# Kernel tuning notes

Measured on AMD Instinct MI355X. Metric: run time of the kernel, lower is better.

The kernel has to match this reference:

```python
import jax, jax.numpy as jnp
import numpy as np

B = 256
N_SNP = 100000
BITS = 4          # snp_onehot_bits
BLOCK = 20        # SNPs per block
N_BLOCKS = N_SNP // BLOCK            # 5000 output blocks
IN_DIM = N_SNP * BITS                # 400000
DIMS = [1024, 256]
OUT_DIM = 1
LN_EPS = 1e-5


def _make_indices():
    # blocks_gt[i] = [20*i, ..., 20*i+19]; replicate get_param4sparse
    blocks = np.arange(N_SNP, dtype=np.int64).reshape(N_BLOCKS, BLOCK)
    idx0 = (blocks[:, :, None] * BITS + np.arange(BITS)).reshape(-1)   # input bit index, [nnz]
    idx1 = np.repeat(np.arange(N_BLOCKS, dtype=np.int64), BLOCK * BITS)  # output block index, [nnz]
    return jnp.asarray(idx0, jnp.int32), jnp.asarray(idx1, jnp.int32)


def setup_inputs() -> dict:
    key = jax.random.key(0)
    ks = jax.random.split(key, 9)
    idx0, idx1 = _make_indices()
    x = jax.random.uniform(ks[0], (B, IN_DIM), dtype=jnp.float32)
    sparse_values = jax.random.normal(ks[1], (idx0.shape[0],), dtype=jnp.float32)
    ln_gamma = jnp.ones((N_BLOCKS,), jnp.float32)
    ln_beta = jnp.zeros((N_BLOCKS,), jnp.float32)
    s1 = 1.0 / np.sqrt(N_BLOCKS)
    W1 = jax.random.uniform(ks[2], (DIMS[0], N_BLOCKS), jnp.float32, -s1, s1)
    b1 = jax.random.uniform(ks[3], (DIMS[0],), jnp.float32, -s1, s1)
    s2 = 1.0 / np.sqrt(DIMS[0])
    W2 = jax.random.uniform(ks[4], (DIMS[1], DIMS[0]), jnp.float32, -s2, s2)
    b2 = jax.random.uniform(ks[5], (DIMS[1],), jnp.float32, -s2, s2)
    s3 = 1.0 / np.sqrt(DIMS[1])
    W3 = jax.random.uniform(ks[6], (OUT_DIM, DIMS[1]), jnp.float32, -s3, s3)
    b3 = jax.random.uniform(ks[7], (OUT_DIM,), jnp.float32, -s3, s3)
    return {"x": x, "sparse_values": sparse_values, "ln_gamma": ln_gamma,
            "ln_beta": ln_beta, "W1": W1, "b1": b1, "W2": W2, "b2": b2,
            "W3": W3, "b3": b3, "idx0": idx0, "idx1": idx1}


def reference(x, sparse_values, ln_gamma, ln_beta, W1, b1, W2, b2, W3, b3, idx0, idx1):
    # SparseLinear: out[b, j] = sum_{k: idx1[k]==j} sparse_values[k] * x[b, idx0[k]]
    gathered = x[:, idx0] * sparse_values[None, :]                       # [B, nnz]
    gblocks = jax.ops.segment_sum(gathered.T, idx1, num_segments=N_BLOCKS).T  # [B, n_blocks]
    # LayerNorm over block dim
    mu = jnp.mean(gblocks, axis=-1, keepdims=True)
    var = jnp.mean(jnp.square(gblocks - mu), axis=-1, keepdims=True)
    h = (gblocks - mu) * jax.lax.rsqrt(var + LN_EPS) * ln_gamma + ln_beta
    # Dense head (note: no activation after first Linear, faithful to source)
    h = h @ W1.T + b1
    h = h @ W2.T + b2
    h = jax.nn.sigmoid(h)
    return h @ W3.T + b3                                                 # [B, OUT_DIM]
```

## Files before the change

kernel.cpp:

```cpp
#include <hip/hip_runtime.h>
#include <math.h>

#define BATCH   256
#define NBLK    5000
#define NBLKP   5024
#define IN_DIM  400000
#define D1      1024
#define D2      256
#define K1P     5120
#define NSPLIT  16
#define ZK      (K1P / NSPLIT)
#define ZSTEPS  (ZK / 64)

typedef __attribute__((ext_vector_type(8))) short short8_t;
typedef __attribute__((ext_vector_type(4))) float f32x4;

static __device__ __forceinline__ unsigned short f2bf(float f) {
    union { float f; unsigned int u; } v; v.f = f;
    unsigned int u = v.u;
    return (unsigned short)((u + 0x7FFFu + ((u >> 16) & 1u)) >> 16);
}

__global__ __launch_bounds__(256) void k_sparse(const float* __restrict__ x,
                                                const float* __restrict__ sv,
                                                float* __restrict__ g) {
    __shared__ float xs[64 * 84];
    const int bx  = blockIdx.x;
    const int b   = blockIdx.y;
    const int tid = threadIdx.x;
    const int gidx = tid >> 2;
    const int s    = tid & 3;
    const int j    = bx * 64 + gidx;
    const bool jv  = (j < NBLK);

    float4 sva[5];
    if (jv) {
        const float4* sr = reinterpret_cast<const float4*>(sv + (size_t)j * 80);
#pragma unroll
        for (int r = 0; r < 5; ++r) sva[r] = sr[r * 4 + s];
    }

    const float* xrow = x + (size_t)b * IN_DIM + (size_t)bx * 5120;
    const int fmax = 100000 - bx * 1280;
#pragma unroll
    for (int i = 0; i < 5; ++i) {
        const int f = tid + i * 256;
        if (f < fmax) {
            const float4 v = *reinterpret_cast<const float4*>(xrow + f * 4);
            const int jl = f / 20;
            const int m  = f % 20;
            *reinterpret_cast<float4*>(&xs[jl * 84 + m * 4]) = v;
        }
    }
    __syncthreads();

    if (!jv) return;
    const float4* xl = reinterpret_cast<const float4*>(&xs[gidx * 84]);
    float acc = 0.0f;
#pragma unroll
    for (int r = 0; r < 5; ++r) {
        const float4 xv = xl[r * 4 + s];
        const float4 sg = sva[r];
        acc += xv.x * sg.x + xv.y * sg.y + xv.z * sg.z + xv.w * sg.w;
    }
    acc += __shfl_xor(acc, 1);
    acc += __shfl_xor(acc, 2);
    if (s == 0) g[(size_t)b * NBLKP + j] = acc;
}

__global__ __launch_bounds__(256) void k_ln(const float* __restrict__ g,
                                            const float* __restrict__ gamma,
                                            const float* __restrict__ beta,
                                            unsigned short* __restrict__ A) {
    const int b   = blockIdx.x;
    const int tid = threadIdx.x;
    const float* row = g + (size_t)b * NBLKP;
    float4 v[5];
    float s = 0.0f, ss = 0.0f;
#pragma unroll
    for (int i = 0; i < 5; ++i) {
        const int f4 = tid + i * 256;
        float4 vv = {0.f, 0.f, 0.f, 0.f};
        if (f4 < 1250) vv = *reinterpret_cast<const float4*>(row + f4 * 4);
        v[i] = vv;
        s  += vv.x + vv.y + vv.z + vv.w;
        ss += vv.x * vv.x + vv.y * vv.y + vv.z * vv.z + vv.w * vv.w;
    }
#pragma unroll
    for (int o = 32; o > 0; o >>= 1) {
        s  += __shfl_xor(s, o);
        ss += __shfl_xor(ss, o);
    }
    __shared__ float ls[4], lss[4];
    const int wid = tid >> 6;
    if ((tid & 63) == 0) { ls[wid] = s; lss[wid] = ss; }
    __syncthreads();
    s  = ls[0] + ls[1] + ls[2] + ls[3];
    ss = lss[0] + lss[1] + lss[2] + lss[3];
    const float mu  = s / (float)NBLK;
    const float var = ss / (float)NBLK - mu * mu;
    const float rs  = rsqrtf(var + 1e-5f);
    unsigned short* dst = A + (size_t)b * K1P;
#pragma unroll
    for (int i = 0; i < 5; ++i) {
        const int f4 = tid + i * 256;
        if (f4 < 1280) {
            const int c = f4 * 4;
            ushort4 o;
            if (f4 < 1250) {
                const float4 gm = *reinterpret_cast<const float4*>(gamma + c);
                const float4 bt = *reinterpret_cast<const float4*>(beta + c);
                o = { f2bf((v[i].x - mu) * rs * gm.x + bt.x),
                      f2bf((v[i].y - mu) * rs * gm.y + bt.y),
                      f2bf((v[i].z - mu) * rs * gm.z + bt.z),
                      f2bf((v[i].w - mu) * rs * gm.w + bt.w) };
            } else {
                o = ushort4{0, 0, 0, 0};
            }
            *reinterpret_cast<ushort4*>(dst + c) = o;
        }
    }
}

__global__ __launch_bounds__(256) void k_gemm1(const unsigned short* __restrict__ A,
                                               const float* __restrict__ W1,
                                               float* __restrict__ C) {
    const int n0 = blockIdx.x * 64;
    const int z  = blockIdx.y;
    const int kbase = z * ZK;
    float* Cz = C + (size_t)z * BATCH * D1;

    __shared__ unsigned short As[256][72];
    __shared__ unsigned short Ws[64][72];

    const int tid  = threadIdx.x;
    const int wave = tid >> 6;
    const int lane = tid & 63;
    const int lr   = lane & 15;
    const int lk   = (lane >> 4) * 8;
    const int srow = tid >> 3;
    const int scol = (tid & 7) * 8;
    const int wrow = tid >> 2;
    const int wcol = (tid & 3) * 16;

    const unsigned short* Ap = A + (size_t)srow * K1P + kbase + scol;
    const float* Wrow = W1 + (size_t)(n0 + wrow) * NBLK;

    short8_t pa[8];
    float4 pwf[4];
    auto loadA = [&](int t) {
#pragma unroll
        for (int it = 0; it < 8; ++it)
            pa[it] = *reinterpret_cast<const short8_t*>(Ap + (size_t)it * 32 * K1P + t * 64);
    };
    auto loadW = [&](int t) {
        const int k0 = kbase + t * 64 + wcol;
#pragma unroll
        for (int q = 0; q < 4; ++q) {
            const int k = k0 + q * 4;
            pwf[q] = (k < NBLK) ? *reinterpret_cast<const float4*>(Wrow + k)
                                : float4{0.f, 0.f, 0.f, 0.f};
        }
    };

    loadA(0);
    loadW(0);

    f32x4 acc[4][4] = {};

    for (int t = 0; t < ZSTEPS; ++t) {
        __syncthreads();
#pragma unroll
        for (int it = 0; it < 8; ++it)
            *reinterpret_cast<short8_t*>(&As[srow + it * 32][scol]) = pa[it];
        {
            short8_t w0 = { (short)f2bf(pwf[0].x), (short)f2bf(pwf[0].y), (short)f2bf(pwf[0].z), (short)f2bf(pwf[0].w),
                            (short)f2bf(pwf[1].x), (short)f2bf(pwf[1].y), (short)f2bf(pwf[1].z), (short)f2bf(pwf[1].w) };
            short8_t w1 = { (short)f2bf(pwf[2].x), (short)f2bf(pwf[2].y), (short)f2bf(pwf[2].z), (short)f2bf(pwf[2].w),
                            (short)f2bf(pwf[3].x), (short)f2bf(pwf[3].y), (short)f2bf(pwf[3].z), (short)f2bf(pwf[3].w) };
            *reinterpret_cast<short8_t*>(&Ws[wrow][wcol])     = w0;
            *reinterpret_cast<short8_t*>(&Ws[wrow][wcol + 8]) = w1;
        }
        __syncthreads();
        if (t + 1 < ZSTEPS) { loadA(t + 1); loadW(t + 1); }
#pragma unroll
        for (int kk = 0; kk < 64; kk += 32) {
            short8_t a[4], bf[4];
#pragma unroll
            for (int i = 0; i < 4; ++i)
                a[i] = *reinterpret_cast<const short8_t*>(&As[wave * 64 + i * 16 + lr][kk + lk]);
#pragma unroll
            for (int jj = 0; jj < 4; ++jj)
                bf[jj] = *reinterpret_cast<const short8_t*>(&Ws[jj * 16 + lr][kk + lk]);
#pragma unroll
            for (int i = 0; i < 4; ++i)
#pragma unroll
                for (int jj = 0; jj < 4; ++jj)
                    acc[i][jj] = __builtin_amdgcn_mfma_f32_16x16x32_bf16(a[i], bf[jj], acc[i][jj], 0, 0, 0);
        }
    }

    const int rbase = (lane >> 4) * 4;
#pragma unroll
    for (int i = 0; i < 4; ++i)
#pragma unroll
        for (int jj = 0; jj < 4; ++jj) {
            const int col = n0 + jj * 16 + lr;
#pragma unroll
            for (int r = 0; r < 4; ++r) {
                const int row = wave * 64 + i * 16 + rbase + r;
                Cz[(size_t)row * D1 + col] = acc[i][jj][r];
            }
        }
}

__global__ __launch_bounds__(256) void k_fuse(const float* __restrict__ p,
                                              const float* __restrict__ b1,
                                              unsigned short* __restrict__ A2,
                                              const float* __restrict__ W2,
                                              unsigned short* __restrict__ W2b) {
    const int idx = (blockIdx.x * 256 + threadIdx.x) * 4;
    const int col = idx & (D1 - 1);
    const size_t S = (size_t)BATCH * D1;
    float4 bb = *reinterpret_cast<const float4*>(b1 + col);
    float sx = bb.x, sy = bb.y, sz = bb.z, sw = bb.w;
#pragma unroll
    for (int q = 0; q < NSPLIT; ++q) {
        float4 v = *reinterpret_cast<const float4*>(p + q * S + idx);
        sx += v.x; sy += v.y; sz += v.z; sw += v.w;
    }
    ushort4 o = { f2bf(sx), f2bf(sy), f2bf(sz), f2bf(sw) };
    *reinterpret_cast<ushort4*>(A2 + idx) = o;
    float4 wv = *reinterpret_cast<const float4*>(W2 + idx);
    ushort4 wo = { f2bf(wv.x), f2bf(wv.y), f2bf(wv.z), f2bf(wv.w) };
    *reinterpret_cast<ushort4*>(W2b + idx) = wo;
}

__global__ __launch_bounds__(512) void k_tail(const unsigned short* __restrict__ A2,
                                              const unsigned short* __restrict__ W2b,
                                              const float* __restrict__ b2,
                                              const float* __restrict__ W3,
                                              const float* __restrict__ b3,
                                              float* __restrict__ out) {
    const int m0 = blockIdx.x * 32;
    __shared__ unsigned short As[32][72];
    __shared__ unsigned short Ws[256][72];
    __shared__ float red[8][32];

    const int tid  = threadIdx.x;
    const int wave = tid >> 6;
    const int lane = tid & 63;
    const int wc   = wave * 32;
    const int lr   = lane & 15;
    const int lk   = (lane >> 4) * 8;
    const int srow = tid >> 3;
    const int scol = (tid & 7) * 8;

    const unsigned short* Ap = A2 + (size_t)(m0 + srow) * D1 + scol;
    const unsigned short* Wp = W2b + (size_t)srow * D1 + scol;

    short8_t pa = {};
    short8_t pw[4];
    if (tid < 256) pa = *reinterpret_cast<const short8_t*>(Ap);
#pragma unroll
    for (int it = 0; it < 4; ++it)
        pw[it] = *reinterpret_cast<const short8_t*>(Wp + (size_t)it * 64 * D1);

    f32x4 acc[2][2] = {};

    for (int t = 0; t < 16; ++t) {
        __syncthreads();
        if (tid < 256) *reinterpret_cast<short8_t*>(&As[srow][scol]) = pa;
#pragma unroll
        for (int it = 0; it < 4; ++it)
            *reinterpret_cast<short8_t*>(&Ws[srow + it * 64][scol]) = pw[it];
        __syncthreads();
        if (t + 1 < 16) {
            const int ko = (t + 1) * 64;
            if (tid < 256) pa = *reinterpret_cast<const short8_t*>(Ap + ko);
#pragma unroll
            for (int it = 0; it < 4; ++it)
                pw[it] = *reinterpret_cast<const short8_t*>(Wp + (size_t)it * 64 * D1 + ko);
        }
#pragma unroll
        for (int kk = 0; kk < 64; kk += 32) {
            short8_t a0 = *reinterpret_cast<const short8_t*>(&As[lr][kk + lk]);
            short8_t a1 = *reinterpret_cast<const short8_t*>(&As[16 + lr][kk + lk]);
#pragma unroll
            for (int j = 0; j < 2; ++j) {
                short8_t bj = *reinterpret_cast<const short8_t*>(&Ws[wc + j * 16 + lr][kk + lk]);
                acc[0][j] = __builtin_amdgcn_mfma_f32_16x16x32_bf16(a0, bj, acc[0][j], 0, 0, 0);
                acc[1][j] = __builtin_amdgcn_mfma_f32_16x16x32_bf16(a1, bj, acc[1][j], 0, 0, 0);
            }
        }
    }

    float b2c[2], w3c[2];
#pragma unroll
    for (int j = 0; j < 2; ++j) {
        const int col = wc + j * 16 + lr;
        b2c[j] = b2[col];
        w3c[j] = W3[col];
    }
    const int rbase = (lane >> 4) * 4;
#pragma unroll
    for (int i = 0; i < 2; ++i) {
#pragma unroll
        for (int r = 0; r < 4; ++r) {
            float pv = 0.0f;
#pragma unroll
            for (int j = 0; j < 2; ++j) {
                const float h = acc[i][j][r] + b2c[j];
                pv += w3c[j] / (1.0f + __expf(-h));
            }
            pv += __shfl_xor(pv, 1);
            pv += __shfl_xor(pv, 2);
            pv += __shfl_xor(pv, 4);
            pv += __shfl_xor(pv, 8);
            if (lr == 0) red[wave][i * 16 + rbase + r] = pv;
        }
    }
    __syncthreads();
    if (tid < 32) {
        float s2 = 0.0f;
#pragma unroll
        for (int w = 0; w < 8; ++w) s2 += red[w][tid];
        out[m0 + tid] = s2 + b3[0];
    }
}

extern "C" void kernel_launch(void* const* d_in, const int* in_sizes, int n_in,
                              void* d_out, int out_size, void* d_ws, size_t ws_size,
                              hipStream_t stream) {
    const float* x     = (const float*)d_in[0];
    const float* sv    = (const float*)d_in[1];
    const float* gamma = (const float*)d_in[2];
    const float* beta  = (const float*)d_in[3];
    const float* W1    = (const float*)d_in[4];
    const float* b1    = (const float*)d_in[5];
    const float* W2    = (const float*)d_in[6];
    const float* b2    = (const float*)d_in[7];
    const float* W3    = (const float*)d_in[8];
    const float* b3    = (const float*)d_in[9];
    float* out = (float*)d_out;

    char* ws = (char*)d_ws;
    size_t off = 0;
    auto alloc = [&](size_t bytes) { char* p = ws + off; off = (off + bytes + 255) & ~(size_t)255; return p; };
    float*          g     = (float*)         alloc((size_t)BATCH * NBLKP * 4);
    unsigned short* Ab    = (unsigned short*)alloc((size_t)BATCH * K1P * 2);
    float*          out1p = (float*)         alloc((size_t)NSPLIT * BATCH * D1 * 4);
    unsigned short* A2b   = (unsigned short*)alloc((size_t)BATCH * D1 * 2);
    unsigned short* W2b   = (unsigned short*)alloc((size_t)D2 * D1 * 2);

    k_sparse<<<dim3((NBLK + 63) / 64, BATCH), 256, 0, stream>>>(x, sv, g);
    k_ln<<<dim3(BATCH), 256, 0, stream>>>(g, gamma, beta, Ab);
    k_gemm1<<<dim3(D1 / 64, NSPLIT), 256, 0, stream>>>(Ab, W1, out1p);
    k_fuse<<<dim3(BATCH * D1 / (256 * 4)), 256, 0, stream>>>(out1p, b1, A2b, W2, W2b);
    k_tail<<<dim3(BATCH / 8), 512, 0, stream>>>(A2b, W2b, b2, W3, b3, out);
}
```

Baseline: 128.5 us.

## Fold LayerNorm algebraically into GEMM1 and drop the separate LN kernel

The separate LayerNorm kernel is removed. k_sparse now emits per-block partial sums and sums of squares. GEMM1 consumes the raw fp32 block outputs, scales W1 by gamma, and accumulates per-column terms sum(gamma*W1) and sum(beta*W1), so the mean and rstd are applied afterwards in k_fuse as rs*(s - mu*t) + u. This saves a kernel launch and a round trip of the normalized activations through memory. The cost is extra gamma/beta loads and conversions inside the GEMM loop, more registers (launch_bounds min 1), and bf16 rounding of raw rather than normalized activations, which may change precision.

```diff
diff --git a/kernel.cpp b/kernel.cpp
--- a/kernel.cpp
+++ b/kernel.cpp
@@ -11,6 +11,7 @@
 #define NSPLIT  16
 #define ZK      (K1P / NSPLIT)
 #define ZSTEPS  (ZK / 64)
+#define NBX     ((NBLK + 63) / 64)
 
 typedef __attribute__((ext_vector_type(8))) short short8_t;
 typedef __attribute__((ext_vector_type(4))) float f32x4;
@@ -20,11 +21,18 @@
     unsigned int u = v.u;
     return (unsigned short)((u + 0x7FFFu + ((u >> 16) & 1u)) >> 16);
 }
+static __device__ __forceinline__ short8_t cvt8(const float4& a, const float4& b) {
+    short8_t r = { (short)f2bf(a.x), (short)f2bf(a.y), (short)f2bf(a.z), (short)f2bf(a.w),
+                   (short)f2bf(b.x), (short)f2bf(b.y), (short)f2bf(b.z), (short)f2bf(b.w) };
+    return r;
+}
 
 __global__ __launch_bounds__(256) void k_sparse(const float* __restrict__ x,
                                                 const float* __restrict__ sv,
-                                                float* __restrict__ g) {
+                                                float* __restrict__ g,
+                                                float2* __restrict__ part) {
     __shared__ float xs[64 * 84];
+    __shared__ float2 pr[4];
     const int bx  = blockIdx.x;
     const int b   = blockIdx.y;
     const int tid = threadIdx.x;
@@ -54,77 +62,43 @@
     }
     __syncthreads();
 
-    if (!jv) return;
-    const float4* xl = reinterpret_cast<const float4*>(&xs[gidx * 84]);
     float acc = 0.0f;
-#pragma unroll
-    for (int r = 0; r < 5; ++r) {
-        const float4 xv = xl[r * 4 + s];
-        const float4 sg = sva[r];
-        acc += xv.x * sg.x + xv.y * sg.y + xv.z * sg.z + xv.w * sg.w;
+    if (jv) {
+        const float4* xl = reinterpret_cast<const float4*>(&xs[gidx * 84]);
+#pragma unroll
+        for (int r = 0; r < 5; ++r) {
+            const float4 xv = xl[r * 4 + s];
+            const float4 sg = sva[r];
+            acc += xv.x * sg.x + xv.y * sg.y + xv.z * sg.z + xv.w * sg.w;
+        }
     }
     acc += __shfl_xor(acc, 1);
     acc += __shfl_xor(acc, 2);
-    if (s == 0) g[(size_t)b * NBLKP + j] = acc;
-}
-
-__global__ __launch_bounds__(256) void k_ln(const float* __restrict__ g,
-                                            const float* __restrict__ gamma,
-                                            const float* __restrict__ beta,
-                                            unsigned short* __restrict__ A) {
-    const int b   = blockIdx.x;
-    const int tid = threadIdx.x;
-    const float* row = g + (size_t)b * NBLKP;
-    float4 v[5];
-    float s = 0.0f, ss = 0.0f;
-#pragma unroll
-    for (int i = 0; i < 5; ++i) {
-        const int f4 = tid + i * 256;
-        float4 vv = {0.f, 0.f, 0.f, 0.f};
-        if (f4 < 1250) vv = *reinterpret_cast<const float4*>(row + f4 * 4);
-        v[i] = vv;
-        s  += vv.x + vv.y + vv.z + vv.w;
-        ss += vv.x * vv.x + vv.y * vv.y + vv.z * vv.z + vv.w * vv.w;
-    }
+    if (s == 0 && jv) g[(size_t)b * NBLKP + j] = acc;
+
+    float sm = (s == 0 && jv) ? acc : 0.0f;
+    float sq = sm * sm;
 #pragma unroll
     for (int o = 32; o > 0; o >>= 1) {
-        s  += __shfl_xor(s, o);
-        ss += __shfl_xor(ss, o);
-    }
-    __shared__ float ls[4], lss[4];
-    const int wid = tid >> 6;
-    if ((tid & 63) == 0) { ls[wid] = s; lss[wid] = ss; }
+        sm += __shfl_xor(sm, o);
+        sq += __shfl_xor(sq, o);
+    }
+    if ((tid & 63) == 0) pr[tid >> 6] = float2{sm, sq};
     __syncthreads();
-    s  = ls[0] + ls[1] + ls[2] + ls[3];
-    ss = lss[0] + lss[1] + lss[2] + lss[3];
-    const float mu  = s / (float)NBLK;
-    const float var = ss / (float)NBLK - mu * mu;
-    const float rs  = rsqrtf(var + 1e-5f);
-    unsigned short* dst = A + (size_t)b * K1P;
-#pragma unroll
-    for (int i = 0; i < 5; ++i) {
-        const int f4 = tid + i * 256;
-        if (f4 < 1280) {
-            const int c = f4 * 4;
-            ushort4 o;
-            if (f4 < 1250) {
-                const float4 gm = *reinterpret_cast<const float4*>(gamma + c);
-                const float4 bt = *reinterpret_cast<const float4*>(beta + c);
-                o = { f2bf((v[i].x - mu) * rs * gm.x + bt.x),
-                      f2bf((v[i].y - mu) * rs * gm.y + bt.y),
-                      f2bf((v[i].z - mu) * rs * gm.z + bt.z),
-                      f2bf((v[i].w - mu) * rs * gm.w + bt.w) };
-            } else {
-                o = ushort4{0, 0, 0, 0};
-            }
-            *reinterpret_cast<ushort4*>(dst + c) = o;
-        }
-    }
-}
-
-__global__ __launch_bounds__(256) void k_gemm1(const unsigned short* __restrict__ A,
-                                               const float* __restrict__ W1,
-                                               float* __restrict__ C) {
+    if (tid == 0) {
+        float2 t = {pr[0].x + pr[1].x + pr[2].x + pr[3].x,
+                    pr[0].y + pr[1].y + pr[2].y + pr[3].y};
+        part[b * 80 + bx] = t;
+    }
+}
+
+__global__ __launch_bounds__(256, 1) void k_gemm1(const float* __restrict__ g,
+                                                  const float* __restrict__ W1,
+                                                  const float* __restrict__ gamma,
+                                                  const float* __restrict__ beta,
+                                                  float* __restrict__ C,
+                                                  float* __restrict__ T1p,
+                                                  float* __restrict__ U1p) {
     const int n0 = blockIdx.x * 64;
     const int z  = blockIdx.y;
     const int kbase = z * ZK;
@@ -143,23 +117,37 @@
     const int wrow = tid >> 2;
     const int wcol = (tid & 3) * 16;
 
-    const unsigned short* Ap = A + (size_t)srow * K1P + kbase + scol;
+    const float* Gp   = g + (size_t)srow * NBLKP + kbase + scol;
     const float* Wrow = W1 + (size_t)(n0 + wrow) * NBLK;
 
-    short8_t pa[8];
-    float4 pwf[4];
+    float4 pa[16];
+    float4 pw[4], pg[4], pb[4];
+
     auto loadA = [&](int t) {
 #pragma unroll
-        for (int it = 0; it < 8; ++it)
-            pa[it] = *reinterpret_cast<const short8_t*>(Ap + (size_t)it * 32 * K1P + t * 64);
+        for (int it = 0; it < 8; ++it) {
+            const int k0 = kbase + t * 64 + scol;
+            const float* base = Gp + (size_t)it * 32 * NBLKP + t * 64;
+            pa[it * 2]     = (k0 < NBLK)     ? *reinterpret_cast<const float4*>(base)
+                                             : float4{0.f, 0.f, 0.f, 0.f};
+            pa[it * 2 + 1] = (k0 + 4 < NBLK) ? *reinterpret_cast<const float4*>(base + 4)
+                                             : float4{0.f, 0.f, 0.f, 0.f};
+        }
     };
     auto loadW = [&](int t) {
         const int k0 = kbase + t * 64 + wcol;
 #pragma unroll
         for (int q = 0; q < 4; ++q) {
             const int k = k0 + q * 4;
-            pwf[q] = (k < NBLK) ? *reinterpret_cast<const float4*>(Wrow + k)
-                                : float4{0.f, 0.f, 0.f, 0.f};
+            if (k < NBLK) {
+                pw[q] = *reinterpret_cast<const float4*>(Wrow + k);
+                pg[q] = *reinterpret_cast<const float4*>(gamma + k);
+                pb[q] = *reinterpret_cast<const float4*>(beta + k);
+            } else {
+                pw[q] = float4{0.f, 0.f, 0.f, 0.f};
+                pg[q] = float4{0.f, 0.f, 0.f, 0.f};
+                pb[q] = float4{0.f, 0.f, 0.f, 0.f};
+            }
         }
     };
 
@@ -167,19 +155,24 @@
     loadW(0);
 
     f32x4 acc[4][4] = {};
+    float t1a = 0.f, u1a = 0.f;
 
     for (int t = 0; t < ZSTEPS; ++t) {
         __syncthreads();
 #pragma unroll
         for (int it = 0; it < 8; ++it)
-            *reinterpret_cast<short8_t*>(&As[srow + it * 32][scol]) = pa[it];
+            *reinterpret_cast<short8_t*>(&As[srow + it * 32][scol]) = cvt8(pa[it * 2], pa[it * 2 + 1]);
         {
-            short8_t w0 = { (short)f2bf(pwf[0].x), (short)f2bf(pwf[0].y), (short)f2bf(pwf[0].z), (short)f2bf(pwf[0].w),
-                            (short)f2bf(pwf[1].x), (short)f2bf(pwf[1].y), (short)f2bf(pwf[1].z), (short)f2bf(pwf[1].w) };
-            short8_t w1 = { (short)f2bf(pwf[2].x), (short)f2bf(pwf[2].y), (short)f2bf(pwf[2].z), (short)f2bf(pwf[2].w),
-                            (short)f2bf(pwf[3].x), (short)f2bf(pwf[3].y), (short)f2bf(pwf[3].z), (short)f2bf(pwf[3].w) };
-            *reinterpret_cast<short8_t*>(&Ws[wrow][wcol])     = w0;
-            *reinterpret_cast<short8_t*>(&Ws[wrow][wcol + 8]) = w1;
+            float4 pr[4];
+#pragma unroll
+            for (int q = 0; q < 4; ++q) {
+                pr[q].x = pg[q].x * pw[q].x; pr[q].y = pg[q].y * pw[q].y;
+                pr[q].z = pg[q].z * pw[q].z; pr[q].w = pg[q].w * pw[q].w;
+                t1a += pr[q].x + pr[q].y + pr[q].z + pr[q].w;
+                u1a += pb[q].x * pw[q].x + pb[q].y * pw[q].y + pb[q].z * pw[q].z + pb[q].w * pw[q].w;
+            }
+            *reinterpret_cast<short8_t*>(&Ws[wrow][wcol])     = cvt8(pr[0], pr[1]);
+            *reinterpret_cast<short8_t*>(&Ws[wrow][wcol + 8]) = cvt8(pr[2], pr[3]);
         }
         __syncthreads();
         if (t + 1 < ZSTEPS) { loadA(t + 1); loadW(t + 1); }
@@ -198,6 +191,13 @@
                 for (int jj = 0; jj < 4; ++jj)
                     acc[i][jj] = __builtin_amdgcn_mfma_f32_16x16x32_bf16(a[i], bf[jj], acc[i][jj], 0, 0, 0);
         }
+    }
+
+    t1a += __shfl_xor(t1a, 1); t1a += __shfl_xor(t1a, 2);
+    u1a += __shfl_xor(u1a, 1); u1a += __shfl_xor(u1a, 2);
+    if ((tid & 3) == 0) {
+        T1p[z * D1 + n0 + wrow] = t1a;
+        U1p[z * D1 + n0 + wrow] = u1a;
     }
 
     const int rbase = (lane >> 4) * 4;
@@ -215,22 +215,52 @@
 }
 
 __global__ __launch_bounds__(256) void k_fuse(const float* __restrict__ p,
+                                              const float2* __restrict__ part,
+                                              const float* __restrict__ T1p,
+                                              const float* __restrict__ U1p,
                                               const float* __restrict__ b1,
                                               unsigned short* __restrict__ A2,
                                               const float* __restrict__ W2,
                                               unsigned short* __restrict__ W2b) {
-    const int idx = (blockIdx.x * 256 + threadIdx.x) * 4;
-    const int col = idx & (D1 - 1);
-    const size_t S = (size_t)BATCH * D1;
+    __shared__ float ls[4], lss[4];
+    const int b   = blockIdx.x;
+    const int tid = threadIdx.x;
+
+    float2 pv = (tid < NBX) ? part[b * 80 + tid] : float2{0.f, 0.f};
+    float sm = pv.x, sq = pv.y;
+#pragma unroll
+    for (int o = 32; o > 0; o >>= 1) {
+        sm += __shfl_xor(sm, o);
+        sq += __shfl_xor(sq, o);
+    }
+    if ((tid & 63) == 0) { ls[tid >> 6] = sm; lss[tid >> 6] = sq; }
+    __syncthreads();
+    const float S  = ls[0] + ls[1] + ls[2] + ls[3];
+    const float SS = lss[0] + lss[1] + lss[2] + lss[3];
+    const float mu = S / (float)NBLK;
+    const float var = SS / (float)NBLK - mu * mu;
+    const float rs  = rsqrtf(var + 1e-5f);
+
+    const int col = tid * 4;
+    const size_t S2 = (size_t)BATCH * D1;
+    float4 s1 = {0.f, 0.f, 0.f, 0.f}, t1 = {0.f, 0.f, 0.f, 0.f}, u1 = {0.f, 0.f, 0.f, 0.f};
+#pragma unroll
+    for (int z = 0; z < NSPLIT; ++z) {
+        float4 v = *reinterpret_cast<const float4*>(p + z * S2 + (size_t)b * D1 + col);
+        s1.x += v.x; s1.y += v.y; s1.z += v.z; s1.w += v.w;
+        float4 tv = *reinterpret_cast<const float4*>(T1p + z * D1 + col);
+        t1.x += tv.x; t1.y += tv.y; t1.z += tv.z; t1.w += tv.w;
+        float4 uv = *reinterpret_cast<const float4*>(U1p + z * D1 + col);
+        u1.x += uv.x; u1.y += uv.y; u1.z += uv.z; u1.w += uv.w;
+    }
     float4 bb = *reinterpret_cast<const float4*>(b1 + col);
-    float sx = bb.x, sy = bb.y, sz = bb.z, sw = bb.w;
-#pragma unroll
-    for (int q = 0; q < NSPLIT; ++q) {
-        float4 v = *reinterpret_cast<const float4*>(p + q * S + idx);
-        sx += v.x; sy += v.y; sz += v.z; sw += v.w;
-    }
-    ushort4 o = { f2bf(sx), f2bf(sy), f2bf(sz), f2bf(sw) };
-    *reinterpret_cast<ushort4*>(A2 + idx) = o;
+    ushort4 o = { f2bf(rs * (s1.x - mu * t1.x) + u1.x + bb.x),
+                  f2bf(rs * (s1.y - mu * t1.y) + u1.y + bb.y),
+                  f2bf(rs * (s1.z - mu * t1.z) + u1.z + bb.z),
+                  f2bf(rs * (s1.w - mu * t1.w) + u1.w + bb.w) };
+    *reinterpret_cast<ushort4*>(A2 + (size_t)b * D1 + col) = o;
+
+    const int idx = b * D1 + col;
     float4 wv = *reinterpret_cast<const float4*>(W2 + idx);
     ushort4 wo = { f2bf(wv.x), f2bf(wv.y), f2bf(wv.z), f2bf(wv.w) };
     *reinterpret_cast<ushort4*>(W2b + idx) = wo;
@@ -348,14 +378,15 @@
     size_t off = 0;
     auto alloc = [&](size_t bytes) { char* p = ws + off; off = (off + bytes + 255) & ~(size_t)255; return p; };
     float*          g     = (float*)         alloc((size_t)BATCH * NBLKP * 4);
-    unsigned short* Ab    = (unsigned short*)alloc((size_t)BATCH * K1P * 2);
+    float2*         part  = (float2*)        alloc((size_t)BATCH * 80 * 8);
     float*          out1p = (float*)         alloc((size_t)NSPLIT * BATCH * D1 * 4);
+    float*          T1p   = (float*)         alloc((size_t)NSPLIT * D1 * 4);
+    float*          U1p   = (float*)         alloc((size_t)NSPLIT * D1 * 4);
     unsigned short* A2b   = (unsigned short*)alloc((size_t)BATCH * D1 * 2);
     unsigned short* W2b   = (unsigned short*)alloc((size_t)D2 * D1 * 2);
 
-    k_sparse<<<dim3((NBLK + 63) / 64, BATCH), 256, 0, stream>>>(x, sv, g);
-    k_ln<<<dim3(BATCH), 256, 0, stream>>>(g, gamma, beta, Ab);
-    k_gemm1<<<dim3(D1 / 64, NSPLIT), 256, 0, stream>>>(Ab, W1, out1p);
-    k_fuse<<<dim3(BATCH * D1 / (256 * 4)), 256, 0, stream>>>(out1p, b1, A2b, W2, W2b);
+    k_sparse<<<dim3(NBX, BATCH), 256, 0, stream>>>(x, sv, g, part);
+    k_gemm1<<<dim3(D1 / 64, NSPLIT), 256, 0, stream>>>(g, W1, gamma, beta, out1p, T1p, U1p);
+    k_fuse<<<dim3(BATCH), 256, 0, stream>>>(out1p, part, T1p, U1p, b1, A2b, W2, W2b);
     k_tail<<<dim3(BATCH / 8), 512, 0, stream>>>(A2b, W2b, b2, W3, b3, out);
 }
```

Result: slower. 133.6 us (+4.0%).

## Fuse LayerNorm, GEMM1, reduction and tail into one persistent kernel with grid barriers

Applied to the files above, without the earlier changes.

Replaces the four kernels after the sparse gather with a single 256-block persistent kernel. Software grid barriers built on atomic counters separate the LayerNorm, split-K GEMM1, partial-sum reduction and the W2/W3 tail phases. The tail is retiled to 32 blocks of 256 threads, each handling 8 rows padded to 16. This removes launch overhead and inter-kernel gaps, but adds a memset and spin barriers. It relies on all 256 blocks being co-resident, and the tail now uses only 32 blocks with half-empty MFMA tiles.

```diff
diff --git a/kernel.cpp b/kernel.cpp
--- a/kernel.cpp
+++ b/kernel.cpp
@@ -11,6 +11,7 @@
 #define NSPLIT  16
 #define ZK      (K1P / NSPLIT)
 #define ZSTEPS  (ZK / 64)
+#define NBX     ((NBLK + 63) / 64)
 
 typedef __attribute__((ext_vector_type(8))) short short8_t;
 typedef __attribute__((ext_vector_type(4))) float f32x4;
@@ -19,6 +20,19 @@
     union { float f; unsigned int u; } v; v.f = f;
     unsigned int u = v.u;
     return (unsigned short)((u + 0x7FFFu + ((u >> 16) & 1u)) >> 16);
+}
+
+static __device__ __forceinline__ void gridbar(unsigned* cnt, unsigned nblk) {
+    __syncthreads();
+    __threadfence();
+    if (threadIdx.x == 0) {
+        __hip_atomic_fetch_add(cnt, 1u, __ATOMIC_ACQ_REL, __HIP_MEMORY_SCOPE_AGENT);
+        while (__hip_atomic_load(cnt, __ATOMIC_ACQUIRE, __HIP_MEMORY_SCOPE_AGENT) < nblk) {
+            __builtin_amdgcn_s_sleep(2);
+        }
+    }
+    __syncthreads();
+    __threadfence();
 }
 
 __global__ __launch_bounds__(256) void k_sparse(const float* __restrict__ x,
@@ -68,264 +82,255 @@
     if (s == 0) g[(size_t)b * NBLKP + j] = acc;
 }
 
-__global__ __launch_bounds__(256) void k_ln(const float* __restrict__ g,
-                                            const float* __restrict__ gamma,
-                                            const float* __restrict__ beta,
-                                            unsigned short* __restrict__ A) {
-    const int b   = blockIdx.x;
+__global__ __launch_bounds__(256) void k_mega(const float* __restrict__ g,
+                                              const float* __restrict__ gamma,
+                                              const float* __restrict__ beta,
+                                              unsigned short* __restrict__ Ab,
+                                              const float* __restrict__ W1,
+                                              float* __restrict__ out1p,
+                                              const float* __restrict__ b1,
+                                              unsigned short* __restrict__ A2b,
+                                              const float* __restrict__ W2,
+                                              unsigned short* __restrict__ W2b,
+                                              const float* __restrict__ b2,
+                                              const float* __restrict__ W3,
+                                              const float* __restrict__ b3,
+                                              float* __restrict__ out,
+                                              unsigned* __restrict__ bars) {
+    __shared__ char smem[47104];
+    const int blk = blockIdx.x;
     const int tid = threadIdx.x;
-    const float* row = g + (size_t)b * NBLKP;
-    float4 v[5];
-    float s = 0.0f, ss = 0.0f;
-#pragma unroll
-    for (int i = 0; i < 5; ++i) {
-        const int f4 = tid + i * 256;
-        float4 vv = {0.f, 0.f, 0.f, 0.f};
-        if (f4 < 1250) vv = *reinterpret_cast<const float4*>(row + f4 * 4);
-        v[i] = vv;
-        s  += vv.x + vv.y + vv.z + vv.w;
-        ss += vv.x * vv.x + vv.y * vv.y + vv.z * vv.z + vv.w * vv.w;
-    }
-#pragma unroll
-    for (int o = 32; o > 0; o >>= 1) {
-        s  += __shfl_xor(s, o);
-        ss += __shfl_xor(ss, o);
-    }
-    __shared__ float ls[4], lss[4];
-    const int wid = tid >> 6;
-    if ((tid & 63) == 0) { ls[wid] = s; lss[wid] = ss; }
-    __syncthreads();
-    s  = ls[0] + ls[1] + ls[2] + ls[3];
-    ss = lss[0] + lss[1] + lss[2] + lss[3];
-    const float mu  = s / (float)NBLK;
-    const float var = ss / (float)NBLK - mu * mu;
-    const float rs  = rsqrtf(var + 1e-5f);
-    unsigned short* dst = A + (size_t)b * K1P;
-#pragma unroll
-    for (int i = 0; i < 5; ++i) {
-        const int f4 = tid + i * 256;
-        if (f4 < 1280) {
-            const int c = f4 * 4;
-            ushort4 o;
-            if (f4 < 1250) {
-                const float4 gm = *reinterpret_cast<const float4*>(gamma + c);
-                const float4 bt = *reinterpret_cast<const float4*>(beta + c);
-                o = { f2bf((v[i].x - mu) * rs * gm.x + bt.x),
-                      f2bf((v[i].y - mu) * rs * gm.y + bt.y),
-                      f2bf((v[i].z - mu) * rs * gm.z + bt.z),
-                      f2bf((v[i].w - mu) * rs * gm.w + bt.w) };
-            } else {
-                o = ushort4{0, 0, 0, 0};
-            }
-            *reinterpret_cast<ushort4*>(dst + c) = o;
-        }
-    }
-}
-
-__global__ __launch_bounds__(256) void k_gemm1(const unsigned short* __restrict__ A,
-                                               const float* __restrict__ W1,
-                                               float* __restrict__ C) {
-    const int n0 = blockIdx.x * 64;
-    const int z  = blockIdx.y;
-    const int kbase = z * ZK;
-    float* Cz = C + (size_t)z * BATCH * D1;
-
-    __shared__ unsigned short As[256][72];
-    __shared__ unsigned short Ws[64][72];
-
-    const int tid  = threadIdx.x;
     const int wave = tid >> 6;
     const int lane = tid & 63;
     const int lr   = lane & 15;
     const int lk   = (lane >> 4) * 8;
-    const int srow = tid >> 3;
-    const int scol = (tid & 7) * 8;
-    const int wrow = tid >> 2;
-    const int wcol = (tid & 3) * 16;
-
-    const unsigned short* Ap = A + (size_t)srow * K1P + kbase + scol;
-    const float* Wrow = W1 + (size_t)(n0 + wrow) * NBLK;
-
-    short8_t pa[8];
-    float4 pwf[4];
-    auto loadA = [&](int t) {
+
+    {
+        float* ls  = (float*)smem;
+        float* lss = ls + 4;
+        const float* row = g + (size_t)blk * NBLKP;
+        float4 v[5];
+        float s = 0.0f, ss = 0.0f;
+#pragma unroll
+        for (int i = 0; i < 5; ++i) {
+            const int f4 = tid + i * 256;
+            float4 vv = {0.f, 0.f, 0.f, 0.f};
+            if (f4 < 1250) vv = *reinterpret_cast<const float4*>(row + f4 * 4);
+            v[i] = vv;
+            s  += vv.x + vv.y + vv.z + vv.w;
+            ss += vv.x * vv.x + vv.y * vv.y + vv.z * vv.z + vv.w * vv.w;
+        }
+#pragma unroll
+        for (int o = 32; o > 0; o >>= 1) {
+            s  += __shfl_xor(s, o);
+            ss += __shfl_xor(ss, o);
+        }
+        if ((tid & 63) == 0) { ls[tid >> 6] = s; lss[tid >> 6] = ss; }
+        __syncthreads();
+        s  = ls[0] + ls[1] + ls[2] + ls[3];
+        ss = lss[0] + lss[1] + lss[2] + lss[3];
+        const float mu  = s / (float)NBLK;
+        const float var = ss / (float)NBLK - mu * mu;
+        const float rs  = rsqrtf(var + 1e-5f);
+        unsigned short* dst = Ab + (size_t)blk * K1P;
+#pragma unroll
+        for (int i = 0; i < 5; ++i) {
+            const int f4 = tid + i * 256;
+            if (f4 < 1280) {
+                const int c = f4 * 4;
+                ushort4 o;
+                if (f4 < 1250) {
+                    const float4 gm = *reinterpret_cast<const float4*>(gamma + c);
+                    const float4 bt = *reinterpret_cast<const float4*>(beta + c);
+                    o = { f2bf((v[i].x - mu) * rs * gm.x + bt.x),
+                          f2bf((v[i].y - mu) * rs * gm.y + bt.y),
+                          f2bf((v[i].z - mu) * rs * gm.z + bt.z),
+                          f2bf((v[i].w - mu) * rs * gm.w + bt.w) };
+                } else {
+                    o = ushort4{0, 0, 0, 0};
+                }
+                *reinterpret_cast<ushort4*>(dst + c) = o;
+            }
+        }
+    }
+    gridbar(&bars[0], 256);
+
+    {
+        const int n0 = (blk & 15) * 64;
+        const int z  = blk >> 4;
+        const int kbase = z * ZK;
+        float* Cz = out1p + (size_t)z * BATCH * D1;
+
+        auto As = (unsigned short(*)[72])smem;
+        auto Ws = (unsigned short(*)[72])(smem + 36864);
+
+        const int srow = tid >> 3;
+        const int scol = (tid & 7) * 8;
+        const int wrow = tid >> 2;
+        const int wcol = (tid & 3) * 16;
+
+        const unsigned short* Ap = Ab + (size_t)srow * K1P + kbase + scol;
+        const float* Wrow = W1 + (size_t)(n0 + wrow) * NBLK;
+
+        short8_t pa[8];
+        float4 pwf[4];
+        auto loadA = [&](int t) {
+#pragma unroll
+            for (int it = 0; it < 8; ++it)
+                pa[it] = *reinterpret_cast<const short8_t*>(Ap + (size_t)it * 32 * K1P + t * 64);
+        };
+        auto loadW = [&](int t) {
+            const int k0 = kbase + t * 64 + wcol;
+#pragma unroll
+            for (int q = 0; q < 4; ++q) {
+                const int k = k0 + q * 4;
+                pwf[q] = (k < NBLK) ? *reinterpret_cast<const float4*>(Wrow + k)
+                                    : float4{0.f, 0.f, 0.f, 0.f};
+            }
+        };
+
+        loadA(0);
+        loadW(0);
+
+        f32x4 acc[4][4] = {};
+
+        for (int t = 0; t < ZSTEPS; ++t) {
+            __syncthreads();
+#pragma unroll
+            for (int it = 0; it < 8; ++it)
+                *reinterpret_cast<short8_t*>(&As[srow + it * 32][scol]) = pa[it];
+            {
+                short8_t w0 = { (short)f2bf(pwf[0].x), (short)f2bf(pwf[0].y), (short)f2bf(pwf[0].z), (short)f2bf(pwf[0].w),
+                                (short)f2bf(pwf[1].x), (short)f2bf(pwf[1].y), (short)f2bf(pwf[1].z), (short)f2bf(pwf[1].w) };
+                short8_t w1 = { (short)f2bf(pwf[2].x), (short)f2bf(pwf[2].y), (short)f2bf(pwf[2].z), (short)f2bf(pwf[2].w),
+                                (short)f2bf(pwf[3].x), (short)f2bf(pwf[3].y), (short)f2bf(pwf[3].z), (short)f2bf(pwf[3].w) };
+                *reinterpret_cast<short8_t*>(&Ws[wrow][wcol])     = w0;
+                *reinterpret_cast<short8_t*>(&Ws[wrow][wcol + 8]) = w1;
+            }
+            __syncthreads();
+            if (t + 1 < ZSTEPS) { loadA(t + 1); loadW(t + 1); }
+#pragma unroll
+            for (int kk = 0; kk < 64; kk += 32) {
+                short8_t a[4], bf[4];
+#pragma unroll
+                for (int i = 0; i < 4; ++i)
+                    a[i] = *reinterpret_cast<const short8_t*>(&As[wave * 64 + i * 16 + lr][kk + lk]);
+#pragma unroll
+                for (int jj = 0; jj < 4; ++jj)
+                    bf[jj] = *reinterpret_cast<const short8_t*>(&Ws[jj * 16 + lr][kk + lk]);
+#pragma unroll
+                for (int i = 0; i < 4; ++i)
+#pragma unroll
+                    for (int jj = 0; jj < 4; ++jj)
+                        acc[i][jj] = __builtin_amdgcn_mfma_f32_16x16x32_bf16(a[i], bf[jj], acc[i][jj], 0, 0, 0);
+            }
+        }
+
+        const int rbase = (lane >> 4) * 4;
+#pragma unroll
+        for (int i = 0; i < 4; ++i)
+#pragma unroll
+            for (int jj = 0; jj < 4; ++jj) {
+                const int col = n0 + jj * 16 + lr;
+#pragma unroll
+                for (int r = 0; r < 4; ++r) {
+                    const int row = wave * 64 + i * 16 + rbase + r;
+                    Cz[(size_t)row * D1 + col] = acc[i][jj][r];
+                }
+            }
+    }
+    gridbar(&bars[1], 256);
+
+    {
+        const int idx = blk * D1 + tid * 4;
+        const int col = tid * 4;
+        const size_t S2 = (size_t)BATCH * D1;
+        float4 bb = *reinterpret_cast<const float4*>(b1 + col);
+        float sx = bb.x, sy = bb.y, sz = bb.z, sw = bb.w;
+#pragma unroll
+        for (int q = 0; q < NSPLIT; ++q) {
+            float4 v = *reinterpret_cast<const float4*>(out1p + q * S2 + idx);
+            sx += v.x; sy += v.y; sz += v.z; sw += v.w;
+        }
+        ushort4 o = { f2bf(sx), f2bf(sy), f2bf(sz), f2bf(sw) };
+        *reinterpret_cast<ushort4*>(A2b + idx) = o;
+        float4 wv = *reinterpret_cast<const float4*>(W2 + idx);
+        ushort4 wo = { f2bf(wv.x), f2bf(wv.y), f2bf(wv.z), f2bf(wv.w) };
+        *reinterpret_cast<ushort4*>(W2b + idx) = wo;
+    }
+    gridbar(&bars[2], 256);
+
+    if (blk < 32) {
+        const int m0 = blk * 8;
+        auto As2 = (unsigned short(*)[72])smem;
+        auto Ws2 = (unsigned short(*)[72])(smem + 2304);
+        float* red = (float*)(smem + 2304 + 36864);
+
+        const int wc = wave * 64;
+        const int srow = tid >> 3;
+        const int scol = (tid & 7) * 8;
+
+        const unsigned short* Wp = W2b + (size_t)srow * D1 + scol;
+        const unsigned short* Ap = A2b + (size_t)(m0 + (tid >> 3)) * D1 + (tid & 7) * 8;
+
+        short8_t pw[8], pa = {};
 #pragma unroll
         for (int it = 0; it < 8; ++it)
-            pa[it] = *reinterpret_cast<const short8_t*>(Ap + (size_t)it * 32 * K1P + t * 64);
-    };
-    auto loadW = [&](int t) {
-        const int k0 = kbase + t * 64 + wcol;
-#pragma unroll
-        for (int q = 0; q < 4; ++q) {
-            const int k = k0 + q * 4;
-            pwf[q] = (k < NBLK) ? *reinterpret_cast<const float4*>(Wrow + k)
-                                : float4{0.f, 0.f, 0.f, 0.f};
-        }
-    };
-
-    loadA(0);
-    loadW(0);
-
-    f32x4 acc[4][4] = {};
-
-    for (int t = 0; t < ZSTEPS; ++t) {
-        __syncthreads();
-#pragma unroll
-        for (int it = 0; it < 8; ++it)
-            *reinterpret_cast<short8_t*>(&As[srow + it * 32][scol]) = pa[it];
-        {
-            short8_t w0 = { (short)f2bf(pwf[0].x), (short)f2bf(pwf[0].y), (short)f2bf(pwf[0].z), (short)f2bf(pwf[0].w),
-                            (short)f2bf(pwf[1].x), (short)f2bf(pwf[1].y), (short)f2bf(pwf[1].z), (short)f2bf(pwf[1].w) };
-            short8_t w1 = { (short)f2bf(pwf[2].x), (short)f2bf(pwf[2].y), (short)f2bf(pwf[2].z), (short)f2bf(pwf[2].w),
-                            (short)f2bf(pwf[3].x), (short)f2bf(pwf[3].y), (short)f2bf(pwf[3].z), (short)f2bf(pwf[3].w) };
-            *reinterpret_cast<short8_t*>(&Ws[wrow][wcol])     = w0;
-            *reinterpret_cast<short8_t*>(&Ws[wrow][wcol + 8]) = w1;
-        }
-        __syncthreads();
-        if (t + 1 < ZSTEPS) { loadA(t + 1); loadW(t + 1); }
-#pragma unroll
-        for (int kk = 0; kk < 64; kk += 32) {
-            short8_t a[4], bf[4];
-#pragma unroll
-            for (int i = 0; i < 4; ++i)
-                a[i] = *reinterpret_cast<const short8_t*>(&As[wave * 64 + i * 16 + lr][kk + lk]);
-#pragma unroll
-            for (int jj = 0; jj < 4; ++jj)
-                bf[jj] = *reinterpret_cast<const short8_t*>(&Ws[jj * 16 + lr][kk + lk]);
-#pragma unroll
-            for (int i = 0; i < 4; ++i)
-#pragma unroll
-                for (int jj = 0; jj < 4; ++jj)
-                    acc[i][jj] = __builtin_amdgcn_mfma_f32_16x16x32_bf16(a[i], bf[jj], acc[i][jj], 0, 0, 0);
-        }
-    }
-
-    const int rbase = (lane >> 4) * 4;
-#pragma unroll
-    for (int i = 0; i < 4; ++i)
-#pragma unroll
-        for (int jj = 0; jj < 4; ++jj) {
-            const int col = n0 + jj * 16 + lr;
-#pragma unroll
-            for (int r = 0; r < 4; ++r) {
-                const int row = wave * 64 + i * 16 + rbase + r;
-                Cz[(size_t)row * D1 + col] = acc[i][jj][r];
-            }
-        }
-}
-
-__global__ __launch_bounds__(256) void k_fuse(const float* __restrict__ p,
-                                              const float* __restrict__ b1,
-                                              unsigned short* __restrict__ A2,
-                                              const float* __restrict__ W2,
-                                              unsigned short* __restrict__ W2b) {
-    const int idx = (blockIdx.x * 256 + threadIdx.x) * 4;
-    const int col = idx & (D1 - 1);
-    const size_t S = (size_t)BATCH * D1;
-    float4 bb = *reinterpret_cast<const float4*>(b1 + col);
-    float sx = bb.x, sy = bb.y, sz = bb.z, sw = bb.w;
-#pragma unroll
-    for (int q = 0; q < NSPLIT; ++q) {
-        float4 v = *reinterpret_cast<const float4*>(p + q * S + idx);
-        sx += v.x; sy += v.y; sz += v.z; sw += v.w;
-    }
-    ushort4 o = { f2bf(sx), f2bf(sy), f2bf(sz), f2bf(sw) };
-    *reinterpret_cast<ushort4*>(A2 + idx) = o;
-    float4 wv = *reinterpret_cast<const float4*>(W2 + idx);
-    ushort4 wo = { f2bf(wv.x), f2bf(wv.y), f2bf(wv.z), f2bf(wv.w) };
-    *reinterpret_cast<ushort4*>(W2b + idx) = wo;
-}
-
-__global__ __launch_bounds__(512) void k_tail(const unsigned short* __restrict__ A2,
-                                              const unsigned short* __restrict__ W2b,
-                                              const float* __restrict__ b2,
-                                              const float* __restrict__ W3,
-                                              const float* __restrict__ b3,
-                                              float* __restrict__ out) {
-    const int m0 = blockIdx.x * 32;
-    __shared__ unsigned short As[32][72];
-    __shared__ unsigned short Ws[256][72];
-    __shared__ float red[8][32];
-
-    const int tid  = threadIdx.x;
-    const int wave = tid >> 6;
-    const int lane = tid & 63;
-    const int wc   = wave * 32;
-    const int lr   = lane & 15;
-    const int lk   = (lane >> 4) * 8;
-    const int srow = tid >> 3;
-    const int scol = (tid & 7) * 8;
-
-    const unsigned short* Ap = A2 + (size_t)(m0 + srow) * D1 + scol;
-    const unsigned short* Wp = W2b + (size_t)srow * D1 + scol;
-
-    short8_t pa = {};
-    short8_t pw[4];
-    if (tid < 256) pa = *reinterpret_cast<const short8_t*>(Ap);
-#pragma unroll
-    for (int it = 0; it < 4; ++it)
-        pw[it] = *reinterpret_cast<const short8_t*>(Wp + (size_t)it * 64 * D1);
-
-    f32x4 acc[2][2] = {};
-
-    for (int t = 0; t < 16; ++t) {
-        __syncthreads();
-        if (tid < 256) *reinterpret_cast<short8_t*>(&As[srow][scol]) = pa;
-#pragma unroll
-        for (int it = 0; it < 4; ++it)
-            *reinterpret_cast<short8_t*>(&Ws[srow + it * 64][scol]) = pw[it];
-        __syncthreads();
-        if (t + 1 < 16) {
-            const int ko = (t + 1) * 64;
-            if (tid < 256) pa = *reinterpret_cast<const short8_t*>(Ap + ko);
-#pragma unroll
-            for (int it = 0; it < 4; ++it)
-                pw[it] = *reinterpret_cast<const short8_t*>(Wp + (size_t)it * 64 * D1 + ko);
-        }
-#pragma unroll
-        for (int kk = 0; kk < 64; kk += 32) {
-            short8_t a0 = *reinterpret_cast<const short8_t*>(&As[lr][kk + lk]);
-            short8_t a1 = *reinterpret_cast<const short8_t*>(&As[16 + lr][kk + lk]);
-#pragma unroll
-            for (int j = 0; j < 2; ++j) {
-                short8_t bj = *reinterpret_cast<const short8_t*>(&Ws[wc + j * 16 + lr][kk + lk]);
-                acc[0][j] = __builtin_amdgcn_mfma_f32_16x16x32_bf16(a0, bj, acc[0][j], 0, 0, 0);
-                acc[1][j] = __builtin_amdgcn_mfma_f32_16x16x32_bf16(a1, bj, acc[1][j], 0, 0, 0);
-            }
-        }
-    }
-
-    float b2c[2], w3c[2];
-#pragma unroll
-    for (int j = 0; j < 2; ++j) {
-        const int col = wc + j * 16 + lr;
-        b2c[j] = b2[col];
-        w3c[j] = W3[col];
-    }
-    const int rbase = (lane >> 4) * 4;
-#pragma unroll
-    for (int i = 0; i < 2; ++i) {
+            pw[it] = *reinterpret_cast<const short8_t*>(Wp + (size_t)it * 32 * D1);
+        if (tid < 64) pa = *reinterpret_cast<const short8_t*>(Ap);
+
+        if (tid < 64) {
+            short8_t zz = {};
+            *reinterpret_cast<short8_t*>(&As2[8 + (tid >> 3)][(tid & 7) * 8]) = zz;
+        }
+
+        f32x4 acc[4] = {};
+        for (int t = 0; t < 16; ++t) {
+            __syncthreads();
+            if (tid < 64) *reinterpret_cast<short8_t*>(&As2[tid >> 3][(tid & 7) * 8]) = pa;
+#pragma unroll
+            for (int it = 0; it < 8; ++it)
+                *reinterpret_cast<short8_t*>(&Ws2[srow + it * 32][scol]) = pw[it];
+            __syncthreads();
+            if (t + 1 < 16) {
+                const int ko = (t + 1) * 64;
+                if (tid < 64) pa = *reinterpret_cast<const short8_t*>(Ap + ko);
+#pragma unroll
+                for (int it = 0; it < 8; ++it)
+                    pw[it] = *reinterpret_cast<const short8_t*>(Wp + (size_t)it * 32 * D1 + ko);
+            }
+#pragma unroll
+            for (int kk = 0; kk < 64; kk += 32) {
+                short8_t a = *reinterpret_cast<const short8_t*>(&As2[lr][kk + lk]);
+#pragma unroll
+                for (int j = 0; j < 4; ++j) {
+                    short8_t bj = *reinterpret_cast<const short8_t*>(&Ws2[wc + j * 16 + lr][kk + lk]);
+                    acc[j] = __builtin_amdgcn_mfma_f32_16x16x32_bf16(a, bj, acc[j], 0, 0, 0);
+                }
+            }
+        }
+
+        const int rbase = (lane >> 4) * 4;
 #pragma unroll
         for (int r = 0; r < 4; ++r) {
             float pv = 0.0f;
 #pragma unroll
-            for (int j = 0; j < 2; ++j) {
-                const float h = acc[i][j][r] + b2c[j];
-                pv += w3c[j] / (1.0f + __expf(-h));
+            for (int j = 0; j < 4; ++j) {
+                const int col = wc + j * 16 + lr;
+                const float h = acc[j][r] + b2[col];
+                pv += W3[col] / (1.0f + __expf(-h));
             }
             pv += __shfl_xor(pv, 1);
             pv += __shfl_xor(pv, 2);
             pv += __shfl_xor(pv, 4);
             pv += __shfl_xor(pv, 8);
-            if (lr == 0) red[wave][i * 16 + rbase + r] = pv;
-        }
-    }
-    __syncthreads();
-    if (tid < 32) {
-        float s2 = 0.0f;
-#pragma unroll
-        for (int w = 0; w < 8; ++w) s2 += red[w][tid];
-        out[m0 + tid] = s2 + b3[0];
+            if (lr == 0) red[wave * 16 + rbase + r] = pv;
+        }
+        __syncthreads();
+        if (tid < 8) {
+            const float s2 = red[tid] + red[16 + tid] + red[32 + tid] + red[48 + tid];
+            out[m0 + tid] = s2 + b3[0];
+        }
     }
 }
 
@@ -352,10 +357,10 @@
     float*          out1p = (float*)         alloc((size_t)NSPLIT * BATCH * D1 * 4);
     unsigned short* A2b   = (unsigned short*)alloc((size_t)BATCH * D1 * 2);
     unsigned short* W2b   = (unsigned short*)alloc((size_t)D2 * D1 * 2);
-
-    k_sparse<<<dim3((NBLK + 63) / 64, BATCH), 256, 0, stream>>>(x, sv, g);
-    k_ln<<<dim3(BATCH), 256, 0, stream>>>(g, gamma, beta, Ab);
-    k_gemm1<<<dim3(D1 / 64, NSPLIT), 256, 0, stream>>>(Ab, W1, out1p);
-    k_fuse<<<dim3(BATCH * D1 / (256 * 4)), 256, 0, stream>>>(out1p, b1, A2b, W2, W2b);
-    k_tail<<<dim3(BATCH / 8), 512, 0, stream>>>(A2b, W2b, b2, W3, b3, out);
-}
+    unsigned*       bars  = (unsigned*)      alloc(256);
+
+    hipMemsetAsync(bars, 0, 256, stream);
+    k_sparse<<<dim3(NBX, BATCH), 256, 0, stream>>>(x, sv, g);
+    k_mega<<<dim3(256), 256, 0, stream>>>(g, gamma, beta, Ab, W1, out1p,
+                                          b1, A2b, W2, W2b, b2, W3, b3, out, bars);
+}
```

After: 269.8 us. 110% more time.
